# Kernel optimization log

Hardware: AMD Instinct MI355X
Metric: run time of the kernel (lower is better)

## Reference

```python
import jax, jax.numpy as jnp
import numpy as np

NUM_CODES = 8192
DIM = 256
TAU = 1.0
KL_WEIGHT = 0.01
COMMIT_WEIGHT = 0.25
B, C, P = 8, 64, 32


def setup_inputs() -> dict:
    key = jax.random.key(0)
    kz, kc = jax.random.split(key)
    z = jax.random.normal(kz, (B, C, P, DIM), dtype=jnp.float32)
    # nn.init.normal_(codebook.weight, std=1/sqrt(dim))
    codebook = jax.random.normal(kc, (NUM_CODES, DIM), dtype=jnp.float32) / jnp.sqrt(jnp.float32(DIM))
    return {"z": z, "codebook": codebook}


def reference(z, codebook):
    Bq, Cq, Pq, D = z.shape
    flat = z.reshape(-1, D)                                  # (N, D)
    logits = flat @ codebook.T                               # (N, num_codes)
    # training path: gumbel-softmax (hard=False), fixed key for determinism
    g = jax.random.gumbel(jax.random.key(42), logits.shape, dtype=logits.dtype)
    soft_one_hot = jax.nn.softmax((logits + g) / TAU, axis=-1)
    z_q = (soft_one_hot @ codebook).reshape(Bq, Cq, Pq, D)
    # KL to uniform prior: sum(qy * log(qy * K + 1e-10))
    log_qy = jax.nn.log_softmax(logits, axis=-1)
    qy = jnp.exp(log_qy)
    kl_loss = KL_WEIGHT * jnp.mean(jnp.sum(qy * jnp.log(qy * NUM_CODES + 1e-10), axis=-1))
    codes = jnp.argmax(logits, axis=-1).reshape(Bq, Cq, Pq)
    commit_loss = COMMIT_WEIGHT * jnp.mean((jax.lax.stop_gradient(z_q) - z) ** 2)
    z_q_st = z + jax.lax.stop_gradient(z_q - z)              # straight-through
    total_loss = commit_loss + kl_loss
    return (z_q_st, total_loss, codes)
```

## Files before the change

kernel.cpp:

```cpp
#include <hip/hip_runtime.h>
#include <stdint.h>
#include <math.h>

#define N_ROWS   16384
#define N_CODES  8192
#define DIMV     256
#define RT       32
#define CK       32
#define NCHUNK   (N_CODES / CK)
#define OUT_ZQ_N ((size_t)N_ROWS * DIMV)
#define OUT_LOSS OUT_ZQ_N
#define OUT_CODE (OUT_ZQ_N + 1)

#define WS_CBHI 0u
#define WS_CBT  4194304u
#define WS_ACC  8388608u
#define WS_NEED (8388608u + 64u)

#define CB1H_OFF  0
#define CBT0_OFF  16896
#define CBT1_OFF  33792
#define BSTRIDE   1056
#define P_OFF     50688
#define P_ROW     80
#define S2B_OFF   53248
#define SKL_OFF   53504
#define TKL_OFF   53760
#define SMEM_BYTES 54016
#define ZT_ROWF   260
#define CAND_OFF  33792

typedef __attribute__((ext_vector_type(8))) short short8;
typedef __attribute__((ext_vector_type(4))) float float4v;

typedef __attribute__((address_space(1))) uint32_t g_u32;
typedef __attribute__((address_space(3))) uint32_t l_u32;

__device__ __forceinline__ void dma16(const void* gsrc, void* ldst) {
  __builtin_amdgcn_global_load_lds((g_u32*)gsrc, (l_u32*)ldst, 16, 0, 0);
}

__device__ __forceinline__ uint32_t rotl32(uint32_t x, int r) {
  return __builtin_rotateleft32(x, (uint32_t)r);
}

__device__ __forceinline__ uint32_t threefry_bits(uint32_t c) {
  const uint32_t k0 = 0u, k1 = 42u;
  const uint32_t k2 = 0x1BD11BDAu ^ k0 ^ k1;
  uint32_t x0 = 0u + k0;
  uint32_t x1 = c + k1;
#define TF_R(r) { x0 += x1; x1 = rotl32(x1, r); x1 ^= x0; }
  TF_R(13) TF_R(15) TF_R(26) TF_R(6)
  x0 += k1; x1 += k2 + 1u;
  TF_R(17) TF_R(29) TF_R(16) TF_R(24)
  x0 += k2; x1 += k0 + 2u;
  TF_R(13) TF_R(15) TF_R(26) TF_R(6)
  x0 += k0; x1 += k1 + 3u;
  TF_R(17) TF_R(29) TF_R(16) TF_R(24)
  x0 += k1; x1 += k2 + 4u;
  TF_R(13) TF_R(15) TF_R(26) TF_R(6)
  x0 += k2; x1 += k0 + 5u;
#undef TF_R
  return x0 ^ x1;
}

__device__ __forceinline__ float gumbel_at_v1(uint32_t idx) {
  uint32_t bits = threefry_bits(idx);
  float u = __uint_as_float((bits >> 9) | 0x3f800000u) - 1.0f;
  u = fmaxf(u, 1.17549435e-38f);
  return -logf(-logf(u));
}

__device__ __forceinline__ unsigned short f2bf(float x) {
  uint32_t u = __float_as_uint(x);
  u += 0x7fffu + ((u >> 16) & 1u);
  return (unsigned short)(u >> 16);
}
__device__ __forceinline__ float bf2f(unsigned short h) {
  return __uint_as_float(((uint32_t)h) << 16);
}

__global__ __launch_bounds__(256)
void vq_prep(const float* __restrict__ cb, char* __restrict__ ws) {
  __shared__ unsigned short lhs[32 * 260];
  const int c = blockIdx.x;
  const int tid = threadIdx.x;
  const int k0 = c * 32;
  unsigned short* cbhi = (unsigned short*)(ws + WS_CBHI);
  unsigned short* cbt  = (unsigned short*)(ws + WS_CBT);
#pragma unroll
  for (int i = 0; i < 8; ++i) {
    int F = tid + i * 256;
    int code = F >> 6, d4 = (F & 63) * 4;
    float4 v = *(const float4*)(cb + (size_t)(k0 + code) * DIMV + d4);
    unsigned short h0 = f2bf(v.x), h1 = f2bf(v.y), h2 = f2bf(v.z), h3 = f2bf(v.w);
    ushort4 hv = {h0, h1, h2, h3};
    *(ushort4*)(cbhi + (size_t)(k0 + code) * DIMV + d4) = hv;
    *(ushort4*)(&lhs[code * 260 + d4]) = hv;
  }
  __syncthreads();
  const int d = tid;
  unsigned short vals[32];
#pragma unroll
  for (int cc = 0; cc < 32; ++cc) vals[cc] = lhs[cc * 260 + d];
  unsigned short* base = cbt + (size_t)c * 8192 + (size_t)d * 32;
#pragma unroll
  for (int j = 0; j < 8; ++j) {
    ushort4 w = {vals[4 * j], vals[4 * j + 1], vals[4 * j + 2], vals[4 * j + 3]};
    *(ushort4*)(base + j * 4) = w;
  }
}

__global__ __launch_bounds__(256, 2)
void vq_main_v2(const float* __restrict__ z, const float* __restrict__ cb,
                float* __restrict__ out, char* __restrict__ ws) {
  __shared__ __align__(16) char sm[SMEM_BYTES];
  const int tid  = threadIdx.x;
  const int wave = tid >> 6;
  const int lane = tid & 63;
  const int quad = lane >> 4;
  const int n    = lane & 15;
  const int mt   = wave & 1;
  const int nt   = wave >> 1;
  const int r0   = blockIdx.x * RT;
  const int myrow = mt * 16 + quad * 4;
  const char* cbhi_b = ws + WS_CBHI;
  const char* cbt_b  = ws + WS_CBT;
  float* wsA = (float*)(ws + WS_ACC);

  {
    float* zts = (float*)sm;
#pragma unroll
    for (int i = 0; i < 8; ++i) {
      int F = tid + i * 256;
      int row = F >> 6, d4 = (F & 63) * 4;
      *(float4*)(zts + row * ZT_ROWF + d4) =
          *(const float4*)(z + (size_t)(r0 + row) * DIMV + d4);
    }
  }
  __syncthreads();
  short8 zhi[8];
  {
    const float* zts = (const float*)sm;
    const int rowl = mt * 16 + n;
#pragma unroll
    for (int ks = 0; ks < 8; ++ks) {
      const float* zp = zts + rowl * ZT_ROWF + ks * 32 + quad * 8;
      float4 f0 = *(const float4*)zp;
      float4 f1 = *(const float4*)(zp + 4);
      zhi[ks][0] = (short)f2bf(f0.x); zhi[ks][1] = (short)f2bf(f0.y);
      zhi[ks][2] = (short)f2bf(f0.z); zhi[ks][3] = (short)f2bf(f0.w);
      zhi[ks][4] = (short)f2bf(f1.x); zhi[ks][5] = (short)f2bf(f1.y);
      zhi[ks][6] = (short)f2bf(f1.z); zhi[ks][7] = (short)f2bf(f1.w);
    }
  }
  __syncthreads();

#pragma unroll
  for (int i = 0; i < 4; ++i) {
    int b = wave * 4 + i;
    dma16(cbhi_b + (size_t)(2 * b) * 512 + (size_t)lane * 16, sm + CB1H_OFF + b * BSTRIDE);
    dma16(cbt_b + (size_t)b * 1024 + (size_t)lane * 16, sm + CBT0_OFF + b * BSTRIDE);
  }

  float skl[4] = {0.f, 0.f, 0.f, 0.f};
  float tkl[4] = {0.f, 0.f, 0.f, 0.f};
  float s2l[4] = {0.f, 0.f, 0.f, 0.f};
  float v1[4], v2[4];
  int   i1[4], i2[4];
  uint32_t idxr[4];
#pragma unroll
  for (int r = 0; r < 4; ++r) {
    v1[r] = -INFINITY; v2[r] = -INFINITY;
    i1[r] = 0x7fffffff; i2[r] = 0x7fffffff;
    idxr[r] = (uint32_t)(r0 + myrow + r) * (uint32_t)N_CODES + (uint32_t)(nt * 16 + n);
  }
  float4v acc2[8];
#pragma unroll
  for (int t = 0; t < 8; ++t) acc2[t] = (float4v){0.f, 0.f, 0.f, 0.f};

  const int kc = nt * 16 + n;
  const char* bbase = sm + CB1H_OFF + (kc >> 1) * BSTRIDE + (kc & 1) * 512 + quad * 16;

  for (int c = 0; c < NCHUNK; ++c) {
    __syncthreads();

    if (c + 1 < NCHUNK) {
#pragma unroll
      for (int i = 0; i < 4; ++i) {
        int b = wave * 4 + i;
        dma16(cbt_b + (size_t)(c + 1) * 16384 + (size_t)b * 1024 + (size_t)lane * 16,
              sm + (((c + 1) & 1) ? CBT1_OFF : CBT0_OFF) + b * BSTRIDE);
      }
    }

    float4v e0 = (float4v){0.f, 0.f, 0.f, 0.f};
    float4v e1 = (float4v){0.f, 0.f, 0.f, 0.f};
#pragma unroll
    for (int ks = 0; ks < 4; ++ks) {
      short8 ba = *(const short8*)(bbase + (2 * ks) * 64);
      short8 bb = *(const short8*)(bbase + (2 * ks + 1) * 64);
      e0 = __builtin_amdgcn_mfma_f32_16x16x32_bf16(zhi[2 * ks], ba, e0, 0, 0, 0);
      e1 = __builtin_amdgcn_mfma_f32_16x16x32_bf16(zhi[2 * ks + 1], bb, e1, 0, 0, 0);
    }
    float4v acc1 = e0 + e1;

    const int codeg0 = c * CK + kc;
#pragma unroll
    for (int r = 0; r < 4; ++r) {
      float l = acc1[r];
      uint32_t bits = threefry_bits(idxr[r]);
      idxr[r] += 32u;
      float u = __uint_as_float((bits >> 9) | 0x3f800000u) - 1.0f;
      float h = u - 1.0f;
      float uu = fmaxf(u, 1.17549435e-38f);
      float t_hw = -0.69314718056f * __log2f(uu);
      float poly = 1.0f + h * (-0.5f + h * (0.33333333f + h * (-0.25f)));
      float t = (h > -0.015625f) ? (-h * poly) : t_hw;
      float e = __expf(l);
      skl[r] += e;
      tkl[r] = fmaf(e, l, tkl[r]);
      bool b1 = l > v1[r];
      bool b2 = l > v2[r];
      v2[r] = b1 ? v1[r] : (b2 ? l : v2[r]);
      i2[r] = b1 ? i1[r] : (b2 ? codeg0 : i2[r]);
      v1[r] = b1 ? l : v1[r];
      i1[r] = b1 ? codeg0 : i1[r];
      float p = e * __builtin_amdgcn_rcpf(t) * 6.1442123533282097e-06f;
      unsigned short ph = f2bf(p);
      s2l[r] += bf2f(ph);
      *(unsigned short*)(sm + P_OFF + (myrow + r) * P_ROW + kc * 2) = ph;
    }
    __syncthreads();

    if (c + 1 < NCHUNK) {
      const size_t k1 = (size_t)(c + 1) * CK;
#pragma unroll
      for (int i = 0; i < 4; ++i) {
        int b = wave * 4 + i;
        dma16(cbhi_b + (k1 + 2 * b) * 512 + (size_t)lane * 16, sm + CB1H_OFF + b * BSTRIDE);
      }
    }

    {
      const char* cbtb = sm + ((c & 1) ? CBT1_OFF : CBT0_OFF);
      short8 pah0 = *(const short8*)(sm + P_OFF + n * P_ROW + quad * 16);
      short8 pah1 = *(const short8*)(sm + P_OFF + (16 + n) * P_ROW + quad * 16);
#pragma unroll
      for (int t = 0; t < 4; ++t) {
        int dt = wave * 4 + t;
        short8 bb = *(const short8*)(cbtb + dt * BSTRIDE + n * 64 + quad * 16);
        acc2[t * 2 + 0] = __builtin_amdgcn_mfma_f32_16x16x32_bf16(pah0, bb, acc2[t * 2 + 0], 0, 0, 0);
        acc2[t * 2 + 1] = __builtin_amdgcn_mfma_f32_16x16x32_bf16(pah1, bb, acc2[t * 2 + 1], 0, 0, 0);
      }
    }
  }

#pragma unroll
  for (int m = 1; m <= 8; m <<= 1) {
#pragma unroll
    for (int r = 0; r < 4; ++r) {
      s2l[r] += __shfl_xor(s2l[r], m);
      skl[r] += __shfl_xor(skl[r], m);
      tkl[r] += __shfl_xor(tkl[r], m);
    }
  }
  if (n == 0) {
    int off = (nt * 32 + myrow) * 4;
    float4 fs = {s2l[0], s2l[1], s2l[2], s2l[3]};
    *(float4*)(sm + S2B_OFF + off) = fs;
    float4 fk = {skl[0], skl[1], skl[2], skl[3]};
    *(float4*)(sm + SKL_OFF + off) = fk;
    float4 ft = {tkl[0], tkl[1], tkl[2], tkl[3]};
    *(float4*)(sm + TKL_OFF + off) = ft;
  }
  {
    float* zts = (float*)sm;
#pragma unroll
    for (int i = 0; i < 8; ++i) {
      int F = tid + i * 256;
      int row = F >> 6, d4 = (F & 63) * 4;
      *(float4*)(zts + row * ZT_ROWF + d4) =
          *(const float4*)(z + (size_t)(r0 + row) * DIMV + d4);
    }
  }
  __syncthreads();

#pragma unroll
  for (int r = 0; r < 4; ++r) {
    char* cbase = sm + CAND_OFF + (myrow + r) * 512 + (nt * 32 + n * 2) * 8;
    *(float*)(cbase + 0) = v1[r];
    *(int*)(cbase + 4)   = i1[r];
    *(float*)(cbase + 8) = v2[r];
    *(int*)(cbase + 12)  = i2[r];
  }
  __syncthreads();

  const float* zts = (const float*)sm;

  if (tid < 32) {
    int r = tid;
    const float* sklb = (const float*)(sm + SKL_OFF);
    const float* tklb = (const float*)(sm + TKL_OFF);
    float S = sklb[r] + sklb[32 + r];
    float T = tklb[r] + tklb[32 + r];
    float klr = T / S - __logf(S) + 9.010913347279288f;
#pragma unroll
    for (int m = 1; m <= 16; m <<= 1) klr += __shfl_xor(klr, m);
    if (r == 0) atomicAdd(&wsA[0], klr);
  }

  if (tid < 64) {
    int r = tid >> 1, h = tid & 1;
    const char* cbase = sm + CAND_OFF + r * 512 + h * 256;
    float bv[8]; int bi8[8];
#pragma unroll
    for (int k = 0; k < 8; ++k) { bv[k] = -INFINITY; bi8[k] = 0x7fffffff; }
    for (int s = 0; s < 32; ++s) {
      float v = *(const float*)(cbase + s * 8);
      int  id = *(const int*)(cbase + s * 8 + 4);
      if ((v > bv[7]) || (v == bv[7] && id < bi8[7])) {
        float cv = v; int ci = id;
#pragma unroll
        for (int k = 0; k < 8; ++k) {
          bool sw = (cv > bv[k]) || (cv == bv[k] && ci < bi8[k]);
          float tv = bv[k]; int ti = bi8[k];
          if (sw) { bv[k] = cv; bi8[k] = ci; cv = tv; ci = ti; }
        }
      }
    }
    float ovv[8]; int ovi[8];
#pragma unroll
    for (int k = 0; k < 8; ++k) {
      ovv[k] = __shfl_xor(bv[k], 1);
      ovi[k] = __shfl_xor(bi8[k], 1);
    }
#pragma unroll
    for (int kk = 0; kk < 8; ++kk) {
      float cv = ovv[kk]; int ci = ovi[kk];
      if ((cv > bv[7]) || (cv == bv[7] && ci < bi8[7])) {
#pragma unroll
        for (int k = 0; k < 8; ++k) {
          bool sw = (cv > bv[k]) || (cv == bv[k] && ci < bi8[k]);
          float tv = bv[k]; int ti = bi8[k];
          if (sw) { bv[k] = cv; bi8[k] = ci; cv = tv; ci = ti; }
        }
      }
    }
    const float* zp = zts + r * ZT_ROWF;
    double best = -1.0e300;
    int bidx = 0x7fffffff;
#pragma unroll
    for (int k = 0; k < 4; ++k) {
      int cidx = bi8[h * 4 + k];
      const float* cp = cb + (size_t)cidx * DIMV;
      double d = 0.0;
      for (int dd = 0; dd < DIMV; dd += 4) {
        float4 zv = *(const float4*)(zp + dd);
        float4 xv = *(const float4*)(cp + dd);
        d += (double)zv.x * xv.x + (double)zv.y * xv.y +
             (double)zv.z * xv.z + (double)zv.w * xv.w;
      }
      if (d > best || (d == best && cidx < bidx)) { best = d; bidx = cidx; }
    }
    double obest = __shfl_xor(best, 1);
    int    obidx = __shfl_xor(bidx, 1);
    bool take = (obest > best) || (obest == best && obidx < bidx);
    int finali = take ? obidx : bidx;
    if (h == 0) out[OUT_CODE + (size_t)(r0 + r)] = (float)finali;
  }

  float invm0[4], invm1[4];
  {
    const float* s2b = (const float*)(sm + S2B_OFF);
#pragma unroll
    for (int e = 0; e < 4; ++e) {
      float Sa = s2b[quad * 4 + e] + s2b[32 + quad * 4 + e];
      float Sb = s2b[16 + quad * 4 + e] + s2b[32 + 16 + quad * 4 + e];
      invm0[e] = 1.0f / Sa;
      invm1[e] = 1.0f / Sb;
    }
  }
  float cpart = 0.f;
#pragma unroll
  for (int t = 0; t < 4; ++t) {
    int dim = (wave * 4 + t) * 16 + n;
#pragma unroll
    for (int ms = 0; ms < 2; ++ms) {
      float4v a = acc2[t * 2 + ms];
#pragma unroll
      for (int e = 0; e < 4; ++e) {
        int row = ms * 16 + quad * 4 + e;
        float q = a[e] * (ms ? invm1[e] : invm0[e]);
        float zv = zts[row * ZT_ROWF + dim];
        float err = q - zv;
        cpart += err * err;
        out[(size_t)(r0 + row) * DIMV + dim] = zv + err;
      }
    }
  }
#pragma unroll
  for (int m = 1; m <= 32; m <<= 1) cpart += __shfl_xor(cpart, m);
  if (lane == 0) atomicAdd(&wsA[1], cpart);
}

#define ZSTRIDE  260
#define CSTRIDE  260
#define PSTRIDE  36
#define RSTRIDE  17

__global__ __launch_bounds__(256, 2)
void vq_main_v1(const float* __restrict__ z, const float* __restrict__ cb,
                float* __restrict__ out, float* __restrict__ ws_acc) {
  __shared__ float zt[RT * ZSTRIDE];
  __shared__ float cbt[CK * CSTRIDE];
  __shared__ float ptile[RT * PSTRIDE];
  __shared__ float redb[RT * RSTRIDE];
  __shared__ float m2s[RT], s2s[RT], scls[RT];

  const int tid = threadIdx.x;
  const int r0  = blockIdx.x * RT;
#pragma unroll
  for (int p = 0; p < 8; ++p) {
    int q = tid + p * 256;
    int i = q >> 6, c4 = (q & 63) * 4;
    *(float4*)(&zt[i * ZSTRIDE + c4]) = *(const float4*)(z + (size_t)(r0 + i) * DIMV + c4);
  }
  if (tid < RT) { m2s[tid] = -INFINITY; s2s[tid] = 0.f; scls[tid] = 0.f; }
  const int tr = tid & 15, tk = tid >> 4, rowg = tid >> 6;
  const int d4 = (tid & 63) * 4;
  float c_m[2][2], c_s[2][2], c_t[2][2];
  int   c_i[2][2];
#pragma unroll
  for (int a = 0; a < 2; ++a)
#pragma unroll
    for (int b = 0; b < 2; ++b) { c_m[a][b] = -INFINITY; c_s[a][b] = 0.f; c_t[a][b] = 0.f; c_i[a][b] = 0; }
  float acc2[8][4];
#pragma unroll
  for (int j = 0; j < 8; ++j)
#pragma unroll
    for (int e = 0; e < 4; ++e) acc2[j][e] = 0.f;
  __syncthreads();
  for (int c = 0; c < NCHUNK; ++c) {
    const int k0 = c * CK;
#pragma unroll
    for (int p = 0; p < 8; ++p) {
      int q = tid + p * 256;
      int i = q >> 6, c4 = (q & 63) * 4;
      *(float4*)(&cbt[i * CSTRIDE + c4]) = *(const float4*)(cb + (size_t)(k0 + i) * DIMV + c4);
    }
    __syncthreads();
    float l00 = 0.f, l01 = 0.f, l10 = 0.f, l11 = 0.f;
    {
      const float* zp0 = &zt[tr * ZSTRIDE];
      const float* zp1 = &zt[(tr + 16) * ZSTRIDE];
      const float* bp0 = &cbt[tk * CSTRIDE];
      const float* bp1 = &cbt[(tk + 16) * CSTRIDE];
#pragma unroll 4
      for (int d = 0; d < DIMV; d += 4) {
        float4 a0 = *(const float4*)(zp0 + d);
        float4 a1 = *(const float4*)(zp1 + d);
        float4 b0 = *(const float4*)(bp0 + d);
        float4 b1 = *(const float4*)(bp1 + d);
        l00 += a0.x*b0.x + a0.y*b0.y + a0.z*b0.z + a0.w*b0.w;
        l01 += a0.x*b1.x + a0.y*b1.y + a0.z*b1.z + a0.w*b1.w;
        l10 += a1.x*b0.x + a1.y*b0.y + a1.z*b0.z + a1.w*b0.w;
        l11 += a1.x*b1.x + a1.y*b1.y + a1.z*b1.z + a1.w*b1.w;
      }
    }
    float lv2[2][2] = {{l00, l01}, {l10, l11}};
    float a2[2][2];
#pragma unroll
    for (int a = 0; a < 2; ++a) {
      int grow = r0 + tr + a * 16;
#pragma unroll
      for (int b = 0; b < 2; ++b) {
        int gk = k0 + tk + b * 16;
        float g  = gumbel_at_v1((uint32_t)grow * (uint32_t)N_CODES + (uint32_t)gk);
        float lv = lv2[a][b];
        a2[a][b] = lv + g;
        if (lv > c_m[a][b]) {
          float sc = expf(c_m[a][b] - lv);
          c_s[a][b] = c_s[a][b] * sc + 1.0f;
          c_t[a][b] = c_t[a][b] * sc + lv;
          c_m[a][b] = lv;
          c_i[a][b] = gk;
        } else {
          float e = expf(lv - c_m[a][b]);
          c_s[a][b] += e;
          c_t[a][b] += e * lv;
        }
      }
    }
    redb[tr * RSTRIDE + tk]        = fmaxf(a2[0][0], a2[0][1]);
    redb[(tr + 16) * RSTRIDE + tk] = fmaxf(a2[1][0], a2[1][1]);
    __syncthreads();
    if (tid < RT) {
      float cm = -INFINITY;
#pragma unroll
      for (int j = 0; j < 16; ++j) cm = fmaxf(cm, redb[tid * RSTRIDE + j]);
      float m2n = fmaxf(m2s[tid], cm);
      scls[tid] = expf(m2s[tid] - m2n);
      m2s[tid]  = m2n;
    }
    __syncthreads();
#pragma unroll
    for (int a = 0; a < 2; ++a) {
      int row = tr + a * 16;
      float m2r = m2s[row];
      float p0 = expf(a2[a][0] - m2r);
      float p1 = expf(a2[a][1] - m2r);
      ptile[row * PSTRIDE + tk]      = p0;
      ptile[row * PSTRIDE + tk + 16] = p1;
      redb[row * RSTRIDE + tk] = p0 + p1;
    }
    __syncthreads();
    if (tid < RT) {
      float ss = 0.f;
#pragma unroll
      for (int j = 0; j < 16; ++j) ss += redb[tid * RSTRIDE + j];
      s2s[tid] = s2s[tid] * scls[tid] + ss;
    }
#pragma unroll
    for (int j = 0; j < 8; ++j) {
      float sc = scls[rowg * 8 + j];
      acc2[j][0] *= sc; acc2[j][1] *= sc; acc2[j][2] *= sc; acc2[j][3] *= sc;
    }
    for (int k4 = 0; k4 < CK; k4 += 4) {
      float4 cb0 = *(const float4*)(&cbt[(k4 + 0) * CSTRIDE + d4]);
      float4 cb1v = *(const float4*)(&cbt[(k4 + 1) * CSTRIDE + d4]);
      float4 cb2 = *(const float4*)(&cbt[(k4 + 2) * CSTRIDE + d4]);
      float4 cb3 = *(const float4*)(&cbt[(k4 + 3) * CSTRIDE + d4]);
#pragma unroll
      for (int j = 0; j < 8; ++j) {
        float4 p4 = *(const float4*)(&ptile[(rowg * 8 + j) * PSTRIDE + k4]);
        acc2[j][0] += p4.x*cb0.x + p4.y*cb1v.x + p4.z*cb2.x + p4.w*cb3.x;
        acc2[j][1] += p4.x*cb0.y + p4.y*cb1v.y + p4.z*cb2.y + p4.w*cb3.y;
        acc2[j][2] += p4.x*cb0.z + p4.y*cb1v.z + p4.z*cb2.z + p4.w*cb3.z;
        acc2[j][3] += p4.x*cb0.w + p4.y*cb1v.w + p4.z*cb2.w + p4.w*cb3.w;
      }
    }
    __syncthreads();
  }
  float* kbuf = cbt;
#pragma unroll
  for (int a = 0; a < 2; ++a) {
    float m0 = c_m[a][0], m1v = c_m[a][1];
    float m, s, t; int bi;
    if (m0 >= m1v) {
      float e = expf(m1v - m0);
      m = m0; s = c_s[a][0] + c_s[a][1] * e; t = c_t[a][0] + c_t[a][1] * e;
    } else {
      float e = expf(m0 - m1v);
      m = m1v; s = c_s[a][0] * e + c_s[a][1]; t = c_t[a][0] * e + c_t[a][1];
    }
    if (m0 > m1v)      bi = c_i[a][0];
    else if (m1v > m0) bi = c_i[a][1];
    else               bi = min(c_i[a][0], c_i[a][1]);
    int row = tr + a * 16;
    kbuf[row * 65 + tk * 4 + 0] = m;
    kbuf[row * 65 + tk * 4 + 1] = s;
    kbuf[row * 65 + tk * 4 + 2] = t;
    kbuf[row * 65 + tk * 4 + 3] = (float)bi;
  }
  __syncthreads();
  if (tid < RT) {
    int r = tid;
    float M = -INFINITY, S = 0.f, T = 0.f, BM = -INFINITY;
    int BI = 0x7fffffff;
    for (int j = 0; j < 16; ++j) {
      float m  = kbuf[r * 65 + j * 4 + 0];
      float s  = kbuf[r * 65 + j * 4 + 1];
      float t  = kbuf[r * 65 + j * 4 + 2];
      int   bi = (int)kbuf[r * 65 + j * 4 + 3];
      if (m <= M) {
        float e = expf(m - M);
        S += s * e; T += t * e;
      } else {
        float e = expf(M - m);
        S = S * e + s; T = T * e + t; M = m;
      }
      if (m > BM || (m == BM && bi < BI)) { BM = m; BI = bi; }
    }
    float kl = logf((float)N_CODES) + T / S - M - logf(S);
    atomicAdd(&ws_acc[0], kl);
    out[OUT_CODE + (size_t)(r0 + r)] = (float)BI;
  }
  float cpart = 0.f;
#pragma unroll
  for (int j = 0; j < 8; ++j) {
    int row  = rowg * 8 + j;
    int grow = r0 + row;
    float inv = 1.0f / s2s[row];
    float4 zv = *(const float4*)(&zt[row * ZSTRIDE + d4]);
    float q0 = acc2[j][0] * inv, q1 = acc2[j][1] * inv;
    float q2 = acc2[j][2] * inv, q3 = acc2[j][3] * inv;
    float e0 = q0 - zv.x, e1 = q1 - zv.y, e2 = q2 - zv.z, e3 = q3 - zv.w;
    cpart += e0*e0 + e1*e1 + e2*e2 + e3*e3;
    float4 o;
    o.x = zv.x + e0; o.y = zv.y + e1; o.z = zv.z + e2; o.w = zv.w + e3;
    *(float4*)(&out[(size_t)grow * DIMV + d4]) = o;
  }
#pragma unroll
  for (int off = 32; off > 0; off >>= 1) cpart += __shfl_down(cpart, off, 64);
  __syncthreads();
  if ((tid & 63) == 0) redb[tid >> 6] = cpart;
  __syncthreads();
  if (tid == 0) {
    float cs = redb[0] + redb[1] + redb[2] + redb[3];
    atomicAdd(&ws_acc[1], cs);
  }
}

__global__ void vq_finalize(const float* __restrict__ ws_acc, float* __restrict__ out) {
  if (threadIdx.x == 0 && blockIdx.x == 0) {
    float kl = 0.01f * (ws_acc[0] / (float)N_ROWS);
    float cm = 0.25f * (ws_acc[1] / (float)OUT_ZQ_N);
    out[OUT_LOSS] = cm + kl;
  }
}

extern "C" void kernel_launch(void* const* d_in, const int* in_sizes, int n_in,
                              void* d_out, int out_size, void* d_ws, size_t ws_size,
                              hipStream_t stream) {
  (void)in_sizes; (void)n_in; (void)out_size;
  const float* z  = (const float*)d_in[0];
  const float* cb = (const float*)d_in[1];
  float* out = (float*)d_out;
  if (ws_size >= (size_t)WS_NEED) {
    char* ws = (char*)d_ws;
    hipMemsetAsync(ws + WS_ACC, 0, 8, stream);
    vq_prep<<<256, 256, 0, stream>>>(cb, ws);
    vq_main_v2<<<N_ROWS / RT, 256, 0, stream>>>(z, cb, out, ws);
    vq_finalize<<<1, 64, 0, stream>>>((const float*)(ws + WS_ACC), out);
  } else {
    float* ws = (float*)d_ws;
    hipMemsetAsync(ws, 0, 8, stream);
    vq_main_v1<<<N_ROWS / RT, 256, 0, stream>>>(z, cb, out, ws);
    vq_finalize<<<1, 64, 0, stream>>>(ws, out);
  }
}
```

Baseline: 711.2 us.

## Single-buffer codebook tile to cut LDS and raise occupancy to four blocks

Drops the double-buffered transposed-codebook LDS tile. Each chunk now loads its own tile into one buffer at the start of the iteration, which shrinks shared memory enough to request four blocks per CU in the launch bounds. It also replaces the polynomial-plus-log Gumbel transform with a plain hardware log clamped away from zero, and reads z straight from global memory in the epilogue instead of staging it in LDS. The trade-offs are less load latency hidden behind the previous chunk's compute and a tighter register budget. Only 512 blocks are launched, so the extra occupancy may be of limited use.

```diff
diff --git a/kernel.cpp b/kernel.cpp
--- a/kernel.cpp
+++ b/kernel.cpp
@@ -18,17 +18,16 @@
 #define WS_NEED (8388608u + 64u)
 
 #define CB1H_OFF  0
-#define CBT0_OFF  16896
-#define CBT1_OFF  33792
+#define CBT_OFF   16896
 #define BSTRIDE   1056
-#define P_OFF     50688
+#define P_OFF     33792
 #define P_ROW     80
-#define S2B_OFF   53248
-#define SKL_OFF   53504
-#define TKL_OFF   53760
-#define SMEM_BYTES 54016
+#define S2B_OFF   36352
+#define SKL_OFF   36608
+#define TKL_OFF   36864
+#define SMEM_BYTES 37120
 #define ZT_ROWF   260
-#define CAND_OFF  33792
+#define CAND_OFF  0
 
 typedef __attribute__((ext_vector_type(8))) short short8;
 typedef __attribute__((ext_vector_type(4))) float float4v;
@@ -111,7 +110,7 @@
   }
 }
 
-__global__ __launch_bounds__(256, 2)
+__global__ __launch_bounds__(256, 4)
 void vq_main_v2(const float* __restrict__ z, const float* __restrict__ cb,
                 float* __restrict__ out, char* __restrict__ ws) {
   __shared__ __align__(16) char sm[SMEM_BYTES];
@@ -160,7 +159,6 @@
   for (int i = 0; i < 4; ++i) {
     int b = wave * 4 + i;
     dma16(cbhi_b + (size_t)(2 * b) * 512 + (size_t)lane * 16, sm + CB1H_OFF + b * BSTRIDE);
-    dma16(cbt_b + (size_t)b * 1024 + (size_t)lane * 16, sm + CBT0_OFF + b * BSTRIDE);
   }
 
   float skl[4] = {0.f, 0.f, 0.f, 0.f};
@@ -185,13 +183,11 @@
   for (int c = 0; c < NCHUNK; ++c) {
     __syncthreads();
 
-    if (c + 1 < NCHUNK) {
-#pragma unroll
-      for (int i = 0; i < 4; ++i) {
-        int b = wave * 4 + i;
-        dma16(cbt_b + (size_t)(c + 1) * 16384 + (size_t)b * 1024 + (size_t)lane * 16,
-              sm + (((c + 1) & 1) ? CBT1_OFF : CBT0_OFF) + b * BSTRIDE);
-      }
+#pragma unroll
+    for (int i = 0; i < 4; ++i) {
+      int b = wave * 4 + i;
+      dma16(cbt_b + (size_t)c * 16384 + (size_t)b * 1024 + (size_t)lane * 16,
+            sm + CBT_OFF + b * BSTRIDE);
     }
 
     float4v e0 = (float4v){0.f, 0.f, 0.f, 0.f};
@@ -212,11 +208,8 @@
       uint32_t bits = threefry_bits(idxr[r]);
       idxr[r] += 32u;
       float u = __uint_as_float((bits >> 9) | 0x3f800000u) - 1.0f;
-      float h = u - 1.0f;
-      float uu = fmaxf(u, 1.17549435e-38f);
-      float t_hw = -0.69314718056f * __log2f(uu);
-      float poly = 1.0f + h * (-0.5f + h * (0.33333333f + h * (-0.25f)));
-      float t = (h > -0.015625f) ? (-h * poly) : t_hw;
+      float t = -0.69314718056f * __log2f(fmaxf(u, 1.17549435e-38f));
+      t = fmaxf(t, 1.0e-10f);
       float e = __expf(l);
       skl[r] += e;
       tkl[r] = fmaf(e, l, tkl[r]);
@@ -243,13 +236,12 @@
     }
 
     {
-      const char* cbtb = sm + ((c & 1) ? CBT1_OFF : CBT0_OFF);
       short8 pah0 = *(const short8*)(sm + P_OFF + n * P_ROW + quad * 16);
       short8 pah1 = *(const short8*)(sm + P_OFF + (16 + n) * P_ROW + quad * 16);
 #pragma unroll
       for (int t = 0; t < 4; ++t) {
         int dt = wave * 4 + t;
-        short8 bb = *(const short8*)(cbtb + dt * BSTRIDE + n * 64 + quad * 16);
+        short8 bb = *(const short8*)(sm + CBT_OFF + dt * BSTRIDE + n * 64 + quad * 16);
         acc2[t * 2 + 0] = __builtin_amdgcn_mfma_f32_16x16x32_bf16(pah0, bb, acc2[t * 2 + 0], 0, 0, 0);
         acc2[t * 2 + 1] = __builtin_amdgcn_mfma_f32_16x16x32_bf16(pah1, bb, acc2[t * 2 + 1], 0, 0, 0);
       }
@@ -274,18 +266,6 @@
     float4 ft = {tkl[0], tkl[1], tkl[2], tkl[3]};
     *(float4*)(sm + TKL_OFF + off) = ft;
   }
-  {
-    float* zts = (float*)sm;
-#pragma unroll
-    for (int i = 0; i < 8; ++i) {
-      int F = tid + i * 256;
-      int row = F >> 6, d4 = (F & 63) * 4;
-      *(float4*)(zts + row * ZT_ROWF + d4) =
-          *(const float4*)(z + (size_t)(r0 + row) * DIMV + d4);
-    }
-  }
-  __syncthreads();
-
 #pragma unroll
   for (int r = 0; r < 4; ++r) {
     char* cbase = sm + CAND_OFF + (myrow + r) * 512 + (nt * 32 + n * 2) * 8;
@@ -295,8 +275,6 @@
     *(int*)(cbase + 12)  = i2[r];
   }
   __syncthreads();
-
-  const float* zts = (const float*)sm;
 
   if (tid < 32) {
     int r = tid;
@@ -347,7 +325,7 @@
         }
       }
     }
-    const float* zp = zts + r * ZT_ROWF;
+    const float* zp = z + (size_t)(r0 + r) * DIMV;
     double best = -1.0e300;
     int bidx = 0x7fffffff;
 #pragma unroll
@@ -392,7 +370,7 @@
       for (int e = 0; e < 4; ++e) {
         int row = ms * 16 + quad * 4 + e;
         float q = a[e] * (ms ? invm1[e] : invm0[e]);
-        float zv = zts[row * ZT_ROWF + dim];
+        float zv = z[(size_t)(r0 + row) * DIMV + dim];
         float err = q - zv;
         cpart += err * err;
         out[(size_t)(r0 + row) * DIMV + dim] = zv + err;
```

New measurement: 706.8 us. About the same (-0.6%).
